# Kernel optimization log

Measured on AMD Instinct MI355X. Metric: run time of the kernel, lower is better.

Reference implementation:

```python
import jax, jax.numpy as jnp
import numpy as np

D_MODEL = 1024
HEADS = 16
D_K = D_MODEL // HEADS
D_FF = 4096
B, S = 4, 2048
EPS = 1e-5


def _layer_norm(x, gamma, beta):
    mu = jnp.mean(x, axis=-1, keepdims=True)
    var = jnp.mean(jnp.square(x - mu), axis=-1, keepdims=True)
    return (x - mu) * jax.lax.rsqrt(var + EPS) * gamma + beta


def setup_inputs() -> dict:
    key = jax.random.key(0)
    ks = jax.random.split(key, 16)
    s_in = 1.0 / np.sqrt(D_MODEL)
    s_ff = 1.0 / np.sqrt(D_FF)
    inp = {
        "x": jax.random.normal(ks[0], (B, S, D_MODEL), dtype=jnp.float32),
        "src_mask": jnp.ones((B, 1, 1, S), dtype=jnp.int32),
        "Wq": jax.random.uniform(ks[1], (D_MODEL, D_MODEL), jnp.float32, -s_in, s_in),
        "bq": jnp.zeros((D_MODEL,), jnp.float32),
        "Wk": jax.random.uniform(ks[2], (D_MODEL, D_MODEL), jnp.float32, -s_in, s_in),
        "bk": jnp.zeros((D_MODEL,), jnp.float32),
        "Wv": jax.random.uniform(ks[3], (D_MODEL, D_MODEL), jnp.float32, -s_in, s_in),
        "bv": jnp.zeros((D_MODEL,), jnp.float32),
        "Wo": jax.random.uniform(ks[4], (D_MODEL, D_MODEL), jnp.float32, -s_in, s_in),
        "bo": jnp.zeros((D_MODEL,), jnp.float32),
        "W1": jax.random.uniform(ks[5], (D_MODEL, D_FF), jnp.float32, -s_in, s_in),
        "b1": jnp.zeros((D_FF,), jnp.float32),
        "W2": jax.random.uniform(ks[6], (D_FF, D_MODEL), jnp.float32, -s_ff, s_ff),
        "b2": jnp.zeros((D_MODEL,), jnp.float32),
        "g1": jnp.ones((D_MODEL,), jnp.float32),
        "be1": jnp.zeros((D_MODEL,), jnp.float32),
        "g2": jnp.ones((D_MODEL,), jnp.float32),
        "be2": jnp.zeros((D_MODEL,), jnp.float32),
    }
    return inp


def reference(x, src_mask, Wq, bq, Wk, bk, Wv, bv, Wo, bo, W1, b1, W2, b2, g1, be1, g2, be2):
    Bn, L, _ = x.shape
    # Self-attention (dropout=0 / eval)
    q = (x @ Wq + bq).reshape(Bn, L, HEADS, D_K).transpose(0, 2, 1, 3)  # [B,H,L,dk]
    k = (x @ Wk + bk).reshape(Bn, L, HEADS, D_K).transpose(0, 2, 1, 3)
    v = (x @ Wv + bv).reshape(Bn, L, HEADS, D_K).transpose(0, 2, 1, 3)
    scores = jnp.einsum("bhqd,bhkd->bhqk", q, k) / np.sqrt(D_K).astype(np.float32)
    scores = jnp.where(src_mask == 0, -jnp.inf, scores)
    attn = jax.nn.softmax(scores, axis=-1)
    out = jnp.einsum("bhqk,bhkd->bhqd", attn, v)
    out = out.transpose(0, 2, 1, 3).reshape(Bn, L, D_MODEL)
    attn_out = out @ Wo + bo
    x = _layer_norm(x + attn_out, g1, be1)
    # FFN
    ffn = jax.nn.relu(x @ W1 + b1) @ W2 + b2
    x = _layer_norm(x + ffn, g2, be2)
    return x
```

## Files before the change

### kernel.cpp

```cpp
#include <hip/hip_runtime.h>
#include <hip/hip_bf16.h>
#include <cstdint>
#include <cstddef>

typedef __bf16 bf16;
typedef __bf16 bf16x8 __attribute__((ext_vector_type(8)));
typedef float  f32x4  __attribute__((ext_vector_type(4)));
typedef unsigned short u16x4 __attribute__((ext_vector_type(4)));
typedef uint32_t u32x4 __attribute__((ext_vector_type(4)));

static constexpr int D_MODEL = 1024;
static constexpr int HEADS   = 16;
static constexpr int D_KH    = 64;
static constexpr int D_FF    = 4096;
static constexpr int BATCH   = 4;
static constexpr int SEQ     = 2048;
static constexpr int MROWS   = BATCH * SEQ;
static constexpr float QSCALE = 0.18033688011f;

#define VMCNT(n) asm volatile("s_waitcnt vmcnt(" #n ")" ::: "memory")
#define LGKM0()                                            \
  do {                                                     \
    asm volatile("s_waitcnt lgkmcnt(0)" ::: "memory");     \
    __builtin_amdgcn_sched_barrier(0);                     \
  } while (0)

__device__ __forceinline__ unsigned short bfbits(float f) {
  return __builtin_bit_cast(unsigned short, (bf16)f);
}
__device__ __forceinline__ float bf2f(unsigned short u) {
  return __builtin_bit_cast(float, (uint32_t)u << 16);
}
__device__ __forceinline__ float bf2f_hi(uint32_t w) {
  return __builtin_bit_cast(float, w & 0xffff0000u);
}
__device__ __forceinline__ float bf2f_lo(uint32_t w) {
  return __builtin_bit_cast(float, w << 16);
}
__device__ __forceinline__ float exp2_raw(float x) {
  float r;
  asm("v_exp_f32 %0, %1" : "=v"(r) : "v"(x));
  return r;
}

__device__ __forceinline__ void gload_lds16(const void* g, void* l) {
  __builtin_amdgcn_global_load_lds(
      (__attribute__((address_space(1))) uint32_t*)(uintptr_t)g,
      (__attribute__((address_space(3))) uint32_t*)(uintptr_t)l, 16, 0, 0);
}

struct PrepArgs {
  const float* x; bf16* xb;
  const int* mask; uint32_t* flags;
  const float* w1; const float* w2; const float* wx[4];
  bf16* w1t; bf16* w2t; bf16* wxt[4];
};
__global__ void k_prep(PrepArgs p) {
  __shared__ float tile[64][65];
  const int t = blockIdx.x;
  if (t < 4096) {
    int i = (t * 256 + threadIdx.x) * 8;
    const float4* q = (const float4*)(p.x + i);
    float4 a = q[0], b = q[1];
    bf16x8 v;
    v[0] = (bf16)a.x; v[1] = (bf16)a.y; v[2] = (bf16)a.z; v[3] = (bf16)a.w;
    v[4] = (bf16)b.x; v[5] = (bf16)b.y; v[6] = (bf16)b.z; v[7] = (bf16)b.w;
    *(bf16x8*)(p.xb + i) = v;
    return;
  }
  if (t == 4096) {
    __shared__ uint32_t sb[4];
    int tid = threadIdx.x;
    if (tid < 4) sb[tid] = 0;
    __syncthreads();
    if (tid < 128) {
      int b = tid >> 5, tt = tid & 31;
      const int4* q = (const int4*)(p.mask + b * SEQ + tt * 64);
      int all = 1;
#pragma unroll
      for (int i = 0; i < 16; ++i) {
        int4 v = q[i];
        all &= v.x & v.y & v.z & v.w;
      }
      if (all) atomicOr(&sb[b], 1u << tt);
    }
    __syncthreads();
    if (tid < 4) p.flags[tid] = sb[tid];
    return;
  }
  int u = t - 4097;
  const float* W;
  bf16* Wt;
  int K, N, k0, n0;
  if (u < 1024) {
    W = p.w1; Wt = p.w1t; K = 1024; N = 4096;
    k0 = (u & 15) * 64; n0 = (u >> 4) * 64;
  } else if (u < 2048) {
    int v = u - 1024;
    W = p.w2; Wt = p.w2t; K = 4096; N = 1024;
    k0 = (v & 63) * 64; n0 = (v >> 6) * 64;
  } else {
    int v = u - 2048;
    int which = v >> 8, vv = v & 255;
    W = p.wx[which]; Wt = p.wxt[which]; K = 1024; N = 1024;
    k0 = (vv & 15) * 64; n0 = (vv >> 4) * 64;
  }
  const int c4 = threadIdx.x & 15, r0 = threadIdx.x >> 4;
#pragma unroll
  for (int i = 0; i < 4; ++i) {
    int r = r0 + i * 16;
    float4 v = *(const float4*)&W[(size_t)(k0 + r) * N + n0 + c4 * 4];
    tile[r][c4 * 4 + 0] = v.x;
    tile[r][c4 * 4 + 1] = v.y;
    tile[r][c4 * 4 + 2] = v.z;
    tile[r][c4 * 4 + 3] = v.w;
  }
  __syncthreads();
  const int ch = threadIdx.x & 15;
#pragma unroll
  for (int i = 0; i < 4; ++i) {
    int rr = (threadIdx.x >> 4) + i * 16;
    u16x4 pk = {bfbits(tile[ch * 4 + 0][rr]), bfbits(tile[ch * 4 + 1][rr]),
                bfbits(tile[ch * 4 + 2][rr]), bfbits(tile[ch * 4 + 3][rr])};
    *(u16x4*)&Wt[(size_t)(n0 + rr) * K + k0 + ch * 4] = pk;
  }
}

enum { EP_RELU = 0, EP_O16 = 1, EP_QKV = 2 };

template <int EPI, int NREP, bool REMAP>
__global__ __launch_bounds__(512, 2) void k_gemm8(
    const bf16* __restrict__ A, const bf16* __restrict__ Bt,
    const float* __restrict__ bias, const float* __restrict__ bias2,
    const float* __restrict__ bias3,
    void* __restrict__ Cout, void* __restrict__ C2, void* __restrict__ C3,
    int N, int K) {
  extern __shared__ char smem[];
  constexpr int BN = NREP * 64;
  constexpr int HB = NREP / 2;
  const int tid = threadIdx.x;
  const int lane = tid & 63;
  const int wid = tid >> 6;
  const int wm = wid >> 2, wn = wid & 3;
  const int l15 = lane & 15, l4 = lane >> 4;
  int bx, by;
  if constexpr (REMAP) {
    const int L = blockIdx.y * 32 + blockIdx.x;
    const int xcd = L & 7, idx = L >> 3;
    bx = (xcd & 3) * 8 + (idx & 7);
    by = (xcd >> 2) * (gridDim.y >> 1) + (idx >> 3);
  } else {
    bx = blockIdx.x;
    by = blockIdx.y;
  }
  const int NI = K >> 7;

  const int c0 = tid, c1 = tid + 512;
  const bf16* baseA0 = A + (size_t)(bx * 256 + (c0 >> 3)) * K + ((c0 & 7) ^ ((c0 >> 3) & 7)) * 8;
  const bf16* baseA1 = A + (size_t)(bx * 256 + (c1 >> 3)) * K + ((c1 & 7) ^ ((c1 >> 3) & 7)) * 8;
  const bf16* baseB0 = Bt + (size_t)(by * BN + (c0 >> 3)) * K + ((c0 & 7) ^ ((c0 >> 3) & 7)) * 8;
  const bf16* baseB1 = Bt + (size_t)(by * BN + (c1 >> 3)) * K + ((c1 & 7) ^ ((c1 >> 3) & 7)) * 8;
  const size_t rowK128 = (size_t)128 * K;

  auto stA = [&](int h, int t, int buf) {
    gload_lds16(baseA0 + h * rowK128 + t * 64, smem + buf * 32768 + h * 16384 + c0 * 16);
    gload_lds16(baseA1 + h * rowK128 + t * 64, smem + buf * 32768 + h * 16384 + c1 * 16);
  };
  auto stB = [&](int h, int t, int buf) {
    gload_lds16(baseB0 + h * rowK128 + t * 64,
                smem + 65536 + buf * (HB * 16384) + h * 16384 + c0 * 16);
    gload_lds16(baseB1 + h * rowK128 + t * 64,
                smem + 65536 + buf * (HB * 16384) + h * 16384 + c1 * 16);
  };

  const int ch0 = (l4 ^ (l15 & 7)) * 16;
  const int ch1 = ((4 + l4) ^ (l15 & 7)) * 16;
  const int aoff = l15 * 128;
  int boffh[NREP];
#pragma unroll
  for (int n = 0; n < NREP; ++n) {
    int rB = wn * (NREP * 16) + n * 16 + l15;
    boffh[n] = (rB >> 7) * 16384 + (rB & 127) * 128;
  }

  f32x4 acc[8][NREP] = {};
  bf16x8 breg[NREP][2];

  stA(0, 0, 0); stA(1, 0, 0); stB(0, 0, 0);
  if constexpr (HB == 2) stB(1, 0, 0);
  stA(0, 1, 1); stA(1, 1, 1); stB(0, 1, 1);
  if constexpr (HB == 2) stB(1, 1, 1);

  for (int i = 0; i < NI; ++i) {
    const int t1 = 2 * i + 1, t2 = 2 * i + 2;
    const bool notfirst = (i > 0), notlast = (i + 1 < NI);
#pragma unroll
    for (int p = 0; p < 8; ++p) {
      const int q = p & 3;
      const char* Ab = smem + (p >> 2) * 32768 + wm * 16384;
      const char* Bb = smem + 65536 + (p >> 2) * (HB * 16384);
      if (p == 0) {
        if (notfirst) {
          stA(0, t1, 1);
          VMCNT(2);
        } else {
          if constexpr (HB == 2) VMCNT(8); else VMCNT(6);
        }
        __builtin_amdgcn_s_barrier();
      } else if (p == 4) {
        if (notlast) {
          stA(0, t2, 0);
          VMCNT(2);
        } else {
          VMCNT(0);
        }
        __builtin_amdgcn_s_barrier();
      }
      if (q == 0) {
#pragma unroll
        for (int n = 0; n < NREP; ++n) {
          breg[n][0] = *(const bf16x8*)(Bb + boffh[n] + ch0);
          breg[n][1] = *(const bf16x8*)(Bb + boffh[n] + ch1);
        }
      }
      bf16x8 a0k0 = *(const bf16x8*)(Ab + (2 * q + 0) * 2048 + aoff + ch0);
      bf16x8 a0k1 = *(const bf16x8*)(Ab + (2 * q + 0) * 2048 + aoff + ch1);
      bf16x8 a1k0 = *(const bf16x8*)(Ab + (2 * q + 1) * 2048 + aoff + ch0);
      bf16x8 a1k1 = *(const bf16x8*)(Ab + (2 * q + 1) * 2048 + aoff + ch1);
      if (p == 1) { if (notfirst) stA(1, t1, 1); }
      else if (p == 2) { if (notfirst) stB(0, t1, 1); }
      else if (p == 3) { if constexpr (HB == 2) { if (notfirst) stB(1, t1, 1); } }
      else if (p == 5) { if (notlast) stA(1, t2, 0); }
      else if (p == 6) { if (notlast) stB(0, t2, 0); }
      else if (p == 7) { if constexpr (HB == 2) { if (notlast) stB(1, t2, 0); } }
      if (p != 0 && p != 4) __builtin_amdgcn_s_barrier();
      LGKM0();
      __builtin_amdgcn_s_setprio(1);
#pragma unroll
      for (int n = 0; n < NREP; ++n) {
        acc[2 * q + 0][n] = __builtin_amdgcn_mfma_f32_16x16x32_bf16(a0k0, breg[n][0], acc[2 * q + 0][n], 0, 0, 0);
        acc[2 * q + 0][n] = __builtin_amdgcn_mfma_f32_16x16x32_bf16(a0k1, breg[n][1], acc[2 * q + 0][n], 0, 0, 0);
        acc[2 * q + 1][n] = __builtin_amdgcn_mfma_f32_16x16x32_bf16(a1k0, breg[n][0], acc[2 * q + 1][n], 0, 0, 0);
        acc[2 * q + 1][n] = __builtin_amdgcn_mfma_f32_16x16x32_bf16(a1k1, breg[n][1], acc[2 * q + 1][n], 0, 0, 0);
      }
      __builtin_amdgcn_s_setprio(0);
      __builtin_amdgcn_s_barrier();
    }
  }

  constexpr int BPM = 1024 / BN;
  float bia[NREP];
#pragma unroll
  for (int n = 0; n < NREP; ++n) {
    int colL = wn * (NREP * 16) + n * 16 + l15;
    if constexpr (EPI == EP_QKV) {
      const int g = by / BPM;
      const float* bp = (g == 0) ? bias : (g == 1 ? bias2 : bias3);
      bia[n] = bp[(by % BPM) * BN + colL];
    } else {
      bia[n] = bias[by * BN + colL];
    }
  }
#pragma unroll
  for (int mf = 0; mf < 8; ++mf) {
    int row0 = bx * 256 + wm * 128 + mf * 16 + l4 * 4;
#pragma unroll
    for (int n = 0; n < NREP; ++n) {
      int colL = wn * (NREP * 16) + n * 16 + l15;
      if constexpr (EPI == EP_QKV) {
        const int g = by / BPM;
        int cc = (by % BPM) * BN + colL;
        if (g == 2) {
          int bidx = row0 >> 11, s0 = row0 & 2047;
          u16x4 pk;
#pragma unroll
          for (int r = 0; r < 4; ++r) pk[r] = bfbits(acc[mf][n][r] + bia[n]);
          *(u16x4*)((bf16*)C3 + (((size_t)bidx * HEADS + (cc >> 6)) * D_KH + (cc & 63)) * SEQ + s0) = pk;
        } else if (g == 0) {
          bf16* dst = (bf16*)Cout;
#pragma unroll
          for (int r = 0; r < 4; ++r)
            dst[(size_t)(row0 + r) * 1024 + cc] = (bf16)((acc[mf][n][r] + bia[n]) * QSCALE);
        } else {
          bf16* dst = (bf16*)C2;
#pragma unroll
          for (int r = 0; r < 4; ++r)
            dst[(size_t)(row0 + r) * 1024 + cc] = (bf16)(acc[mf][n][r] + bia[n]);
        }
      } else {
        int col = by * BN + colL;
#pragma unroll
        for (int r = 0; r < 4; ++r) {
          float v = acc[mf][n][r] + bia[n];
          if constexpr (EPI == EP_RELU) v = fmaxf(v, 0.f);
          ((bf16*)Cout)[(size_t)(row0 + r) * N + col] = (bf16)v;
        }
      }
    }
  }
}

__global__ __launch_bounds__(256, 4) void k_attn(
    const bf16* __restrict__ Q, const bf16* __restrict__ Kb,
    const bf16* __restrict__ Vt, const int* __restrict__ mask,
    const uint32_t* __restrict__ Mf, bf16* __restrict__ O) {
  __shared__ bf16 Ks[2][64 * 64];
  __shared__ bf16 Vs[2][64 * 64];
  const int tid = threadIdx.x;
  const int lane = tid & 63;
  const int l15 = lane & 15, l4 = lane >> 4;
  const int L = blockIdx.x;
  const int xcd = L & 7, rest = L >> 3;
  const int qx = rest & 15, yhi = rest >> 4;
  const int bh = yhi * 8 + xcd;
  const int b = bh >> 4, h = bh & 15;
  const size_t qrow0 = (size_t)b * SEQ + qx * 128 + (tid >> 6) * 32;
  const bf16* Kbase = Kb + (size_t)b * SEQ * D_MODEL + h * 64;
  const bf16* Vbase = Vt + (size_t)bh * D_KH * SEQ;
  const int* mbase = mask + b * SEQ;
  const uint32_t mflags = Mf[b];

  bf16x8 qf[2][2];
#pragma unroll
  for (int m = 0; m < 2; ++m)
#pragma unroll
    for (int ks = 0; ks < 2; ++ks)
      qf[m][ks] = *(const bf16x8*)&Q[(qrow0 + m * 16 + l15) * D_MODEL + h * 64 + ks * 32 + l4 * 8];

  f32x4 o[2][4] = {};
  f32x4 rs[2] = {};
  bf16x8 ones;
#pragma unroll
  for (int i = 0; i < 8; ++i) ones[i] = (bf16)1.0f;

  const int koff0 = l15 * 64 + ((l4 * 8) ^ ((l15 & 7) << 3));
  const int koff1 = l15 * 64 + ((32 + l4 * 8) ^ ((l15 & 7) << 3));

  const int r0_ = tid >> 3, c0_ = (tid & 7) ^ (r0_ & 7);
  const int o1_ = tid + 256;
  const int r1_ = o1_ >> 3, c1_ = (o1_ & 7) ^ (r1_ & 7);
  const bf16* gK0 = Kbase + (size_t)r0_ * D_MODEL + c0_ * 8;
  const bf16* gK1 = Kbase + (size_t)r1_ * D_MODEL + c1_ * 8;
  const bf16* gV0 = Vbase + (size_t)r0_ * SEQ + c0_ * 8;
  const bf16* gV1 = Vbase + (size_t)r1_ * SEQ + c1_ * 8;
  char* ldsK = (char*)&Ks[0][0] + tid * 16;
  char* ldsV = (char*)&Vs[0][0] + tid * 16;

  auto stage = [&](int buf) {
    gload_lds16(gK0, ldsK + buf * 8192);
    gload_lds16(gK1, ldsK + buf * 8192 + 4096);
    gload_lds16(gV0, ldsV + buf * 8192);
    gload_lds16(gV1, ldsV + buf * 8192 + 4096);
    gK0 += 64 * D_MODEL; gK1 += 64 * D_MODEL;
    gV0 += 64; gV1 += 64;
  };

  stage(0);
  __syncthreads();

  for (int kv0 = 0; kv0 < SEQ; kv0 += 64) {
    const int cur = (kv0 >> 6) & 1;
    if (kv0 + 64 < SEQ) stage(cur ^ 1);
    const bf16* Kc = &Ks[cur][0];
    const bf16* Vc = &Vs[cur][0];

    f32x4 sf[2][4] = {};
    __builtin_amdgcn_s_setprio(1);
#pragma unroll
    for (int ks = 0; ks < 2; ++ks)
#pragma unroll
      for (int n = 0; n < 4; ++n) {
        bf16x8 kf = *(const bf16x8*)&Kc[(ks ? koff1 : koff0) + n * 1024];
#pragma unroll
        for (int m = 0; m < 2; ++m)
          sf[m][n] = __builtin_amdgcn_mfma_f32_16x16x32_bf16(kf, qf[m][ks], sf[m][n], 0, 0, 0);
      }
    __builtin_amdgcn_s_setprio(0);

    if (__builtin_expect(!((mflags >> (kv0 >> 6)) & 1), 0)) {
#pragma unroll
      for (int n = 0; n < 4; ++n) {
        int4 mk = *(const int4*)&mbase[kv0 + n * 16 + l4 * 4];
#pragma unroll
        for (int r = 0; r < 4; ++r)
          if (((const int*)&mk)[r] == 0) {
            sf[0][n][r] = -1e30f;
            sf[1][n][r] = -1e30f;
          }
      }
    }

    uint32_t pk[2][4][2];
#pragma unroll
    for (int m = 0; m < 2; ++m) {
#pragma unroll
      for (int n = 0; n < 4; ++n) {
#pragma unroll
        for (int r = 0; r < 4; ++r) sf[m][n][r] = exp2_raw(sf[m][n][r]);
        asm("v_cvt_pk_bf16_f32 %0, %1, %2"
            : "=v"(pk[m][n][0]) : "v"(sf[m][n][0]), "v"(sf[m][n][1]));
        asm("v_cvt_pk_bf16_f32 %0, %1, %2"
            : "=v"(pk[m][n][1]) : "v"(sf[m][n][2]), "v"(sf[m][n][3]));
      }
    }

    bf16x8 pa[2][2];
#pragma unroll
    for (int m = 0; m < 2; ++m)
#pragma unroll
      for (int ks = 0; ks < 2; ++ks) {
        u32x4 w;
#pragma unroll
        for (int hh = 0; hh < 2; ++hh) {
          uint32_t a = pk[m][ks * 2 + 0][hh];
          uint32_t bsw = pk[m][ks * 2 + 1][hh];
          asm("v_permlane32_swap_b32 %0, %1" : "+v"(a), "+v"(bsw));
          asm("v_permlane16_swap_b32 %0, %1" : "+v"(a), "+v"(bsw));
          w[hh] = a;
          w[2 + hh] = bsw;
        }
        pa[ks][m] = __builtin_bit_cast(bf16x8, w);
      }

#pragma unroll
    for (int ks = 0; ks < 2; ++ks) {
      __builtin_amdgcn_s_setprio(1);
#pragma unroll
      for (int n = 0; n < 4; ++n) {
        bf16x8 vf = *(const bf16x8*)&Vc[(ks ? koff1 : koff0) + n * 1024];
#pragma unroll
        for (int m = 0; m < 2; ++m)
          o[m][n] = __builtin_amdgcn_mfma_f32_16x16x32_bf16(pa[ks][m], vf, o[m][n], 0, 0, 0);
      }
#pragma unroll
      for (int m = 0; m < 2; ++m)
        rs[m] = __builtin_amdgcn_mfma_f32_16x16x32_bf16(pa[ks][m], ones, rs[m], 0, 0, 0);
      __builtin_amdgcn_s_setprio(0);
    }
    __syncthreads();
  }

#pragma unroll
  for (int m = 0; m < 2; ++m) {
    float inv[4];
#pragma unroll
    for (int r = 0; r < 4; ++r) inv[r] = 1.0f / rs[m][r];
#pragma unroll
    for (int n = 0; n < 4; ++n)
#pragma unroll
      for (int r = 0; r < 4; ++r)
        O[(qrow0 + m * 16 + l4 * 4 + r) * D_MODEL + h * 64 + n * 16 + l15] =
            (bf16)(o[m][n][r] * inv[r]);
  }
}

template <bool F32OUT>
__global__ __launch_bounds__(256) void k_add_ln(
    const bf16* __restrict__ a, const bf16* __restrict__ b,
    const float* __restrict__ g, const float* __restrict__ be,
    void* __restrict__ y) {
  const int lane = threadIdx.x & 63;
  const size_t row = (size_t)blockIdx.x * 4 + (threadIdx.x >> 6);
  const size_t base = row * D_MODEL + lane * 16;
  uint4 a0 = *(const uint4*)(a + base);
  uint4 a1 = *(const uint4*)(a + base + 8);
  uint4 b0 = *(const uint4*)(b + base);
  uint4 b1 = *(const uint4*)(b + base + 8);
  float v[16];
  const uint32_t* pa0 = (const uint32_t*)&a0;
  const uint32_t* pb0 = (const uint32_t*)&b0;
  const uint32_t* pa1 = (const uint32_t*)&a1;
  const uint32_t* pb1 = (const uint32_t*)&b1;
#pragma unroll
  for (int i = 0; i < 4; ++i) {
    v[2 * i + 0] = bf2f_lo(pa0[i]) + bf2f_lo(pb0[i]);
    v[2 * i + 1] = bf2f_hi(pa0[i]) + bf2f_hi(pb0[i]);
    v[8 + 2 * i + 0] = bf2f_lo(pa1[i]) + bf2f_lo(pb1[i]);
    v[8 + 2 * i + 1] = bf2f_hi(pa1[i]) + bf2f_hi(pb1[i]);
  }
  float s = 0.f, s2 = 0.f;
#pragma unroll
  for (int i = 0; i < 16; ++i) {
    s += v[i];
    s2 = fmaf(v[i], v[i], s2);
  }
#pragma unroll
  for (int off = 1; off < 64; off <<= 1) {
    s  += __shfl_xor(s, off);
    s2 += __shfl_xor(s2, off);
  }
  float mu  = s * (1.f / D_MODEL);
  float var = s2 * (1.f / D_MODEL) - mu * mu;
  float rstd = rsqrtf(var + 1e-5f);
  const float4* gp = (const float4*)(g + lane * 16);
  const float4* bp = (const float4*)(be + lane * 16);
#pragma unroll
  for (int i = 0; i < 4; ++i) {
    float4 gg = gp[i], bb = bp[i];
    float y0 = (v[4 * i + 0] - mu) * rstd * gg.x + bb.x;
    float y1 = (v[4 * i + 1] - mu) * rstd * gg.y + bb.y;
    float y2 = (v[4 * i + 2] - mu) * rstd * gg.z + bb.z;
    float y3 = (v[4 * i + 3] - mu) * rstd * gg.w + bb.w;
    if constexpr (F32OUT) {
      *(float4*)((float*)y + base + 4 * i) = make_float4(y0, y1, y2, y3);
    } else {
      u16x4 pk = {bfbits(y0), bfbits(y1), bfbits(y2), bfbits(y3)};
      *(u16x4*)((bf16*)y + base + 4 * i) = pk;
    }
  }
}

extern "C" void kernel_launch(void* const* d_in, const int* in_sizes, int n_in,
                              void* d_out, int out_size, void* d_ws, size_t ws_size,
                              hipStream_t stream) {
  const float* x   = (const float*)d_in[0];
  const int*  mask = (const int*)d_in[1];
  const float* Wq  = (const float*)d_in[2];
  const float* bq  = (const float*)d_in[3];
  const float* Wk  = (const float*)d_in[4];
  const float* bk_ = (const float*)d_in[5];
  const float* Wv  = (const float*)d_in[6];
  const float* bv  = (const float*)d_in[7];
  const float* Wo  = (const float*)d_in[8];
  const float* bo  = (const float*)d_in[9];
  const float* W1  = (const float*)d_in[10];
  const float* b1  = (const float*)d_in[11];
  const float* W2  = (const float*)d_in[12];
  const float* b2  = (const float*)d_in[13];
  const float* g1  = (const float*)d_in[14];
  const float* be1 = (const float*)d_in[15];
  const float* g2  = (const float*)d_in[16];
  const float* be2 = (const float*)d_in[17];

  char* ws = (char*)d_ws;
  const size_t MB = 1ull << 20;
  bf16*  xb    = (bf16*)(ws + 0);
  bf16*  Qb    = (bf16*)(ws + 16 * MB);
  bf16*  Kbuf  = (bf16*)(ws + 32 * MB);
  bf16*  Vt    = (bf16*)(ws + 48 * MB);
  bf16*  Hb    = (bf16*)(ws + 0);
  bf16*  aproj = (bf16*)(ws + 64 * MB);
  bf16*  f2o   = (bf16*)(ws + 80 * MB);
  bf16*  Ob    = (bf16*)(ws + 96 * MB);
  uint32_t* mfl = (uint32_t*)(ws + 112 * MB);
  bf16*  x1b   = (bf16*)(ws + 128 * MB);
  bf16*  Wqkvt = (bf16*)(ws + 144 * MB);
  bf16*  Wot   = (bf16*)(ws + 150 * MB);
  bf16*  W1t   = (bf16*)(ws + 152 * MB);
  bf16*  W2t   = (bf16*)(ws + 160 * MB);

  const int SM4 = 131072, SM2 = 98304;
  hipFuncSetAttribute(reinterpret_cast<const void*>(&k_gemm8<EP_QKV, 2, true>),
                      hipFuncAttributeMaxDynamicSharedMemorySize, SM2);
  hipFuncSetAttribute(reinterpret_cast<const void*>(&k_gemm8<EP_RELU, 4, true>),
                      hipFuncAttributeMaxDynamicSharedMemorySize, SM4);
  hipFuncSetAttribute(reinterpret_cast<const void*>(&k_gemm8<EP_O16, 2, true>),
                      hipFuncAttributeMaxDynamicSharedMemorySize, SM2);
  hipFuncSetAttribute(reinterpret_cast<const void*>(&k_gemm8<EP_O16, 2, false>),
                      hipFuncAttributeMaxDynamicSharedMemorySize, SM2);

  PrepArgs pp;
  pp.x = x; pp.xb = xb; pp.mask = mask; pp.flags = mfl;
  pp.w1 = W1; pp.w1t = W1t;
  pp.w2 = W2; pp.w2t = W2t;
  pp.wx[0] = Wq; pp.wxt[0] = Wqkvt;
  pp.wx[1] = Wk; pp.wxt[1] = Wqkvt + 1024 * 1024;
  pp.wx[2] = Wv; pp.wxt[2] = Wqkvt + 2 * 1024 * 1024;
  pp.wx[3] = Wo; pp.wxt[3] = Wot;
  k_prep<<<7169, 256, 0, stream>>>(pp);

  k_gemm8<EP_QKV, 2, true><<<dim3(32, 24), 512, SM2, stream>>>(
      xb, Wqkvt, bq, bk_, bv, Qb, Kbuf, Vt, 3072, 1024);

  k_attn<<<1024, 256, 0, stream>>>(Qb, Kbuf, Vt, mask, mfl, Ob);

  k_gemm8<EP_O16, 2, false><<<dim3(32, 8), 512, SM2, stream>>>(
      Ob, Wot, bo, nullptr, nullptr, aproj, nullptr, nullptr, 1024, 1024);
  k_add_ln<false><<<MROWS / 4, 256, 0, stream>>>(xb, aproj, g1, be1, x1b);

  k_gemm8<EP_RELU, 4, true><<<dim3(32, 16), 512, SM4, stream>>>(
      x1b, W1t, b1, nullptr, nullptr, Hb, nullptr, nullptr, 4096, 1024);
  k_gemm8<EP_O16, 2, true><<<dim3(32, 8), 512, SM2, stream>>>(
      Hb, W2t, b2, nullptr, nullptr, f2o, nullptr, nullptr, 1024, 4096);
  k_add_ln<true><<<MROWS / 4, 256, 0, stream>>>(x1b, f2o, g2, be2, (float*)d_out);
}
```

Before: 332.4 us.

## Double attention query tile per block and drop GEMM XCD block remapping

The attention kernel now gives each wave 64 query rows instead of 32, so each block covers 256 queries and the grid shrinks from 1024 to 512 blocks. Each K/V tile loaded into LDS is therefore reused across twice as many queries, and the V fragments are hoisted into registers once per tile instead of being reloaded per query group. The extra accumulators raise register pressure, so occupancy is relaxed to 2 blocks per CU, which may reduce latency hiding. Separately, the XCD-aware block remapping in the GEMM kernels is removed in favour of plain blockIdx ordering, which could change L2 locality.

```diff
diff --git a/kernel.cpp b/kernel.cpp
--- a/kernel.cpp
+++ b/kernel.cpp
@@ -128,7 +128,7 @@
 
 enum { EP_RELU = 0, EP_O16 = 1, EP_QKV = 2 };
 
-template <int EPI, int NREP, bool REMAP>
+template <int EPI, int NREP>
 __global__ __launch_bounds__(512, 2) void k_gemm8(
     const bf16* __restrict__ A, const bf16* __restrict__ Bt,
     const float* __restrict__ bias, const float* __restrict__ bias2,
@@ -143,16 +143,7 @@
   const int wid = tid >> 6;
   const int wm = wid >> 2, wn = wid & 3;
   const int l15 = lane & 15, l4 = lane >> 4;
-  int bx, by;
-  if constexpr (REMAP) {
-    const int L = blockIdx.y * 32 + blockIdx.x;
-    const int xcd = L & 7, idx = L >> 3;
-    bx = (xcd & 3) * 8 + (idx & 7);
-    by = (xcd >> 2) * (gridDim.y >> 1) + (idx >> 3);
-  } else {
-    bx = blockIdx.x;
-    by = blockIdx.y;
-  }
+  const int bx = blockIdx.x, by = blockIdx.y;
   const int NI = K >> 7;
 
   const int c0 = tid, c1 = tid + 512;
@@ -300,7 +291,7 @@
   }
 }
 
-__global__ __launch_bounds__(256, 4) void k_attn(
+__global__ __launch_bounds__(256, 2) void k_attn(
     const bf16* __restrict__ Q, const bf16* __restrict__ Kb,
     const bf16* __restrict__ Vt, const int* __restrict__ mask,
     const uint32_t* __restrict__ Mf, bf16* __restrict__ O) {
@@ -311,24 +302,24 @@
   const int l15 = lane & 15, l4 = lane >> 4;
   const int L = blockIdx.x;
   const int xcd = L & 7, rest = L >> 3;
-  const int qx = rest & 15, yhi = rest >> 4;
+  const int qx = rest & 7, yhi = rest >> 3;
   const int bh = yhi * 8 + xcd;
   const int b = bh >> 4, h = bh & 15;
-  const size_t qrow0 = (size_t)b * SEQ + qx * 128 + (tid >> 6) * 32;
+  const size_t qrow0 = (size_t)b * SEQ + qx * 256 + (tid >> 6) * 64;
   const bf16* Kbase = Kb + (size_t)b * SEQ * D_MODEL + h * 64;
   const bf16* Vbase = Vt + (size_t)bh * D_KH * SEQ;
   const int* mbase = mask + b * SEQ;
   const uint32_t mflags = Mf[b];
 
-  bf16x8 qf[2][2];
-#pragma unroll
-  for (int m = 0; m < 2; ++m)
+  bf16x8 qf[4][2];
+#pragma unroll
+  for (int m = 0; m < 4; ++m)
 #pragma unroll
     for (int ks = 0; ks < 2; ++ks)
       qf[m][ks] = *(const bf16x8*)&Q[(qrow0 + m * 16 + l15) * D_MODEL + h * 64 + ks * 32 + l4 * 8];
 
-  f32x4 o[2][4] = {};
-  f32x4 rs[2] = {};
+  f32x4 o[4][4] = {};
+  f32x4 rs[4] = {};
   bf16x8 ones;
 #pragma unroll
   for (int i = 0; i < 8; ++i) ones[i] = (bf16)1.0f;
@@ -364,7 +355,7 @@
     const bf16* Kc = &Ks[cur][0];
     const bf16* Vc = &Vs[cur][0];
 
-    f32x4 sf[2][4] = {};
+    f32x4 sf[4][4] = {};
     __builtin_amdgcn_s_setprio(1);
 #pragma unroll
     for (int ks = 0; ks < 2; ++ks)
@@ -372,7 +363,7 @@
       for (int n = 0; n < 4; ++n) {
         bf16x8 kf = *(const bf16x8*)&Kc[(ks ? koff1 : koff0) + n * 1024];
 #pragma unroll
-        for (int m = 0; m < 2; ++m)
+        for (int m = 0; m < 4; ++m)
           sf[m][n] = __builtin_amdgcn_mfma_f32_16x16x32_bf16(kf, qf[m][ks], sf[m][n], 0, 0, 0);
       }
     __builtin_amdgcn_s_setprio(0);
@@ -384,64 +375,61 @@
 #pragma unroll
         for (int r = 0; r < 4; ++r)
           if (((const int*)&mk)[r] == 0) {
-            sf[0][n][r] = -1e30f;
-            sf[1][n][r] = -1e30f;
+#pragma unroll
+            for (int m = 0; m < 4; ++m) sf[m][n][r] = -1e30f;
           }
       }
     }
 
-    uint32_t pk[2][4][2];
-#pragma unroll
-    for (int m = 0; m < 2; ++m) {
+    bf16x8 vf[2][4];
+#pragma unroll
+    for (int ks = 0; ks < 2; ++ks)
+#pragma unroll
+      for (int n = 0; n < 4; ++n)
+        vf[ks][n] = *(const bf16x8*)&Vc[(ks ? koff1 : koff0) + n * 1024];
+
+#pragma unroll
+    for (int m = 0; m < 4; ++m) {
+      uint32_t pk[4][2];
 #pragma unroll
       for (int n = 0; n < 4; ++n) {
 #pragma unroll
         for (int r = 0; r < 4; ++r) sf[m][n][r] = exp2_raw(sf[m][n][r]);
         asm("v_cvt_pk_bf16_f32 %0, %1, %2"
-            : "=v"(pk[m][n][0]) : "v"(sf[m][n][0]), "v"(sf[m][n][1]));
+            : "=v"(pk[n][0]) : "v"(sf[m][n][0]), "v"(sf[m][n][1]));
         asm("v_cvt_pk_bf16_f32 %0, %1, %2"
-            : "=v"(pk[m][n][1]) : "v"(sf[m][n][2]), "v"(sf[m][n][3]));
-      }
-    }
-
-    bf16x8 pa[2][2];
-#pragma unroll
-    for (int m = 0; m < 2; ++m)
+            : "=v"(pk[n][1]) : "v"(sf[m][n][2]), "v"(sf[m][n][3]));
+      }
+      bf16x8 pa[2];
 #pragma unroll
       for (int ks = 0; ks < 2; ++ks) {
         u32x4 w;
 #pragma unroll
         for (int hh = 0; hh < 2; ++hh) {
-          uint32_t a = pk[m][ks * 2 + 0][hh];
-          uint32_t bsw = pk[m][ks * 2 + 1][hh];
+          uint32_t a = pk[ks * 2 + 0][hh];
+          uint32_t bsw = pk[ks * 2 + 1][hh];
           asm("v_permlane32_swap_b32 %0, %1" : "+v"(a), "+v"(bsw));
           asm("v_permlane16_swap_b32 %0, %1" : "+v"(a), "+v"(bsw));
           w[hh] = a;
           w[2 + hh] = bsw;
         }
-        pa[ks][m] = __builtin_bit_cast(bf16x8, w);
-      }
-
-#pragma unroll
-    for (int ks = 0; ks < 2; ++ks) {
+        pa[ks] = __builtin_bit_cast(bf16x8, w);
+      }
       __builtin_amdgcn_s_setprio(1);
 #pragma unroll
-      for (int n = 0; n < 4; ++n) {
-        bf16x8 vf = *(const bf16x8*)&Vc[(ks ? koff1 : koff0) + n * 1024];
-#pragma unroll
-        for (int m = 0; m < 2; ++m)
-          o[m][n] = __builtin_amdgcn_mfma_f32_16x16x32_bf16(pa[ks][m], vf, o[m][n], 0, 0, 0);
-      }
-#pragma unroll
-      for (int m = 0; m < 2; ++m)
-        rs[m] = __builtin_amdgcn_mfma_f32_16x16x32_bf16(pa[ks][m], ones, rs[m], 0, 0, 0);
+      for (int ks = 0; ks < 2; ++ks) {
+#pragma unroll
+        for (int n = 0; n < 4; ++n)
+          o[m][n] = __builtin_amdgcn_mfma_f32_16x16x32_bf16(pa[ks], vf[ks][n], o[m][n], 0, 0, 0);
+        rs[m] = __builtin_amdgcn_mfma_f32_16x16x32_bf16(pa[ks], ones, rs[m], 0, 0, 0);
+      }
       __builtin_amdgcn_s_setprio(0);
     }
     __syncthreads();
   }
 
 #pragma unroll
-  for (int m = 0; m < 2; ++m) {
+  for (int m = 0; m < 4; ++m) {
     float inv[4];
 #pragma unroll
     for (int r = 0; r < 4; ++r) inv[r] = 1.0f / rs[m][r];
@@ -550,13 +538,11 @@
   bf16*  W2t   = (bf16*)(ws + 160 * MB);
 
   const int SM4 = 131072, SM2 = 98304;
-  hipFuncSetAttribute(reinterpret_cast<const void*>(&k_gemm8<EP_QKV, 2, true>),
+  hipFuncSetAttribute(reinterpret_cast<const void*>(&k_gemm8<EP_QKV, 2>),
                       hipFuncAttributeMaxDynamicSharedMemorySize, SM2);
-  hipFuncSetAttribute(reinterpret_cast<const void*>(&k_gemm8<EP_RELU, 4, true>),
+  hipFuncSetAttribute(reinterpret_cast<const void*>(&k_gemm8<EP_RELU, 4>),
                       hipFuncAttributeMaxDynamicSharedMemorySize, SM4);
-  hipFuncSetAttribute(reinterpret_cast<const void*>(&k_gemm8<EP_O16, 2, true>),
-                      hipFuncAttributeMaxDynamicSharedMemorySize, SM2);
-  hipFuncSetAttribute(reinterpret_cast<const void*>(&k_gemm8<EP_O16, 2, false>),
+  hipFuncSetAttribute(reinterpret_cast<const void*>(&k_gemm8<EP_O16, 2>),
                       hipFuncAttributeMaxDynamicSharedMemorySize, SM2);
 
   PrepArgs pp;
@@ -569,18 +555,18 @@
   pp.wx[3] = Wo; pp.wxt[3] = Wot;
   k_prep<<<7169, 256, 0, stream>>>(pp);
 
-  k_gemm8<EP_QKV, 2, true><<<dim3(32, 24), 512, SM2, stream>>>(
+  k_gemm8<EP_QKV, 2><<<dim3(32, 24), 512, SM2, stream>>>(
       xb, Wqkvt, bq, bk_, bv, Qb, Kbuf, Vt, 3072, 1024);
 
-  k_attn<<<1024, 256, 0, stream>>>(Qb, Kbuf, Vt, mask, mfl, Ob);
-
-  k_gemm8<EP_O16, 2, false><<<dim3(32, 8), 512, SM2, stream>>>(
+  k_attn<<<512, 256, 0, stream>>>(Qb, Kbuf, Vt, mask, mfl, Ob);
+
+  k_gemm8<EP_O16, 2><<<dim3(32, 8), 512, SM2, stream>>>(
       Ob, Wot, bo, nullptr, nullptr, aproj, nullptr, nullptr, 1024, 1024);
   k_add_ln<false><<<MROWS / 4, 256, 0, stream>>>(xb, aproj, g1, be1, x1b);
 
-  k_gemm8<EP_RELU, 4, true><<<dim3(32, 16), 512, SM4, stream>>>(
+  k_gemm8<EP_RELU, 4><<<dim3(32, 16), 512, SM4, stream>>>(
       x1b, W1t, b1, nullptr, nullptr, Hb, nullptr, nullptr, 4096, 1024);
-  k_gemm8<EP_O16, 2, true><<<dim3(32, 8), 512, SM2, stream>>>(
+  k_gemm8<EP_O16, 2><<<dim3(32, 8), 512, SM2, stream>>>(
       Hb, W2t, b2, nullptr, nullptr, f2o, nullptr, nullptr, 1024, 4096);
   k_add_ln<true><<<MROWS / 4, 256, 0, stream>>>(x1b, f2o, g2, be2, (float*)d_out);
 }
```

After: 322.7 us. 1.03x faster.
